# Optimization experiments

Measured on AMD Instinct MI355X. Metric: run time of the kernel, lower is better.

Reference implementation:

```python
import jax, jax.numpy as jnp
import numpy as np


def _layernorm(x, g, b, eps=1e-6):
    mu = jnp.mean(x, -1, keepdims=True)
    var = jnp.var(x, -1, keepdims=True)
    return (x - mu) * jax.lax.rsqrt(var + eps) * g + b


def _rope_interleave(x, cos, sin):
    # de-interleave pairs (x0,x1),(x2,x3),... -> [evens | odds]  (matches
    # torch view(..., d//2, 2).transpose(-1,-2).reshape(..., d))
    x = jnp.concatenate([x[..., 0::2], x[..., 1::2]], axis=-1)
    d = x.shape[-1]
    x1, x2 = x[..., : d // 2], x[..., d // 2 :]
    rot = jnp.concatenate([-x2, x1], axis=-1)
    return x * cos + rot * sin


def setup_inputs() -> dict:
    key = jax.random.key(0)
    k = jax.random.split(key, 6)
    T, H, D, R, HID, QLR, K = 2048, 32, 128, 64, 4096, 1536, 256
    hidden_states = jax.random.normal(k[0], (1, T, HID), jnp.float32)
    q_latent = jax.random.normal(k[1], (1, T, QLR), jnp.float32)
    wq_b = jax.random.normal(k[2], (QLR, H * D), jnp.float32) * 0.02
    wk = jax.random.normal(k[3], (HID, D), jnp.float32) * 0.02
    w_proj = jax.random.normal(k[4], (HID, H), jnp.float32) * 0.02
    k_gamma = jnp.ones((D,), jnp.float32)
    k_beta = jnp.zeros((D,), jnp.float32)
    # real rotary cos/sin tables for the 64-dim rope slice
    pos = jnp.arange(T, dtype=jnp.float32)
    inv_freq = 1.0 / (10000.0 ** (jnp.arange(0, R, 2, dtype=jnp.float32) / R))
    freqs = jnp.outer(pos, inv_freq)
    emb = jnp.concatenate([freqs, freqs], axis=-1)  # [T, R]
    cos, sin = jnp.cos(emb), jnp.sin(emb)
    ks = jnp.zeros((T,), jnp.int32)
    ke = jnp.arange(1, T + 1, dtype=jnp.int32)  # causal: keys [0, t]
    return dict(hidden_states=hidden_states, q_latent=q_latent, ks=ks, ke=ke,
                cos=cos, sin=sin, wq_b=wq_b, wk=wk, k_gamma=k_gamma,
                k_beta=k_beta, w_proj=w_proj, index_topk=K)


def reference(hidden_states, q_latent, ks, ke, cos, sin, wq_b, wk,
              k_gamma, k_beta, w_proj, index_topk):
    T = hidden_states.shape[1]
    H = w_proj.shape[1]
    D = wk.shape[1]
    R = cos.shape[-1]
    weight_scale = (D ** -0.5) * (H ** -0.5)

    q = (q_latent[0] @ wq_b).reshape(T, H, D)              # [T,H,D]
    k = _layernorm(hidden_states[0] @ wk, k_gamma, k_beta)  # [T,D]
    w = hidden_states[0] @ w_proj                           # [T,H]

    q_pe = _rope_interleave(q[..., :R], cos[:, None, :], sin[:, None, :])
    k_pe = _rope_interleave(k[..., :R], cos, sin)
    q = jnp.concatenate([q_pe, q[..., R:]], axis=-1)
    k = jnp.concatenate([k_pe, k[..., R:]], axis=-1)

    # lightning-indexer score: I[t,s] = sum_h w[t,h] * relu(q[t,h] . k[s])
    scores = jnp.einsum('thd,sd->ths', q, k)                # [T,H,S]
    scores = jnp.einsum('ths,th->ts', jax.nn.relu(scores), w) * weight_scale

    j = jnp.arange(T)
    mask = (j[None, :] >= ks[:, None]) & (j[None, :] < ke[:, None])
    scores = jnp.where(mask, scores, -1e30)
    values, idx = jax.lax.top_k(scores, index_topk)
    return idx.reshape(1, T, 1, index_topk), values
```

## Files before the change

### kernel.cpp

```cpp
#include <hip/hip_runtime.h>
#include <cstdint>

typedef unsigned short u16;
typedef unsigned int   u32;
typedef unsigned long long u64;

typedef short bf16x8 __attribute__((ext_vector_type(8)));
typedef float f32x4  __attribute__((ext_vector_type(4)));
typedef u16   u16x8  __attribute__((ext_vector_type(8)));

__device__ __forceinline__ u16 f2b(float f){
  u32 u = __float_as_uint(f);
  u += 0x7FFFu + ((u >> 16) & 1u);
  return (u16)(u >> 16);
}
__device__ __forceinline__ float b2f(u16 h){ return __uint_as_float(((u32)h) << 16); }
__device__ __forceinline__ u32 fkey(float f){
  u32 u = __float_as_uint(f);
  return u ^ ((u & 0x80000000u) ? 0xFFFFFFFFu : 0x80000000u);
}
__device__ __forceinline__ float unkey(u32 k){
  u32 u = (k & 0x80000000u) ? (k ^ 0x80000000u) : ~k;
  return __uint_as_float(u);
}
__device__ __forceinline__ void gload16(const void* g, void* l){
  __builtin_amdgcn_global_load_lds(
      reinterpret_cast<const __attribute__((address_space(1))) char*>(reinterpret_cast<uintptr_t>(g)),
      reinterpret_cast<__attribute__((address_space(3))) char*>(reinterpret_cast<uintptr_t>(l)),
      16, 0, 0);
}

__global__ __launch_bounds__(256) void k_init(const int* __restrict__ ke, int* __restrict__ list){
  __shared__ int km[64];
  int tid = threadIdx.x;
  if (tid < 64){
    int m = 0;
    for (int j = 0; j < 32; j++) m = max(m, ke[tid * 32 + j]);
    km[tid] = m;
  }
  __syncthreads();
  if (tid < 8){
    int x = tid, n = 0;
    for (int j0 = 0; j0 < 8; j0++){
      int tb = j0 * 8 + x;
      int kmax = km[tb];
      for (int sb = 0; sb < 16; sb++){
        if (sb * 128 < kmax){
          list[n * 8 + x] = tb * 32 + sb * 2 + 0; n++;
          list[n * 8 + x] = tb * 32 + sb * 2 + 1; n++;
        }
      }
    }
    for (; n < 256; n++) list[n * 8 + x] = -1;
  }
}

__global__ __launch_bounds__(256) void k_cvt(const float* __restrict__ in, u16* __restrict__ out, int n8){
  int i = blockIdx.x * 256 + threadIdx.x;
  if (i >= n8) return;
  const float4* p = (const float4*)in + (size_t)i * 2;
  float4 a = p[0], b = p[1];
  u16x8 v;
  v[0]=f2b(a.x); v[1]=f2b(a.y); v[2]=f2b(a.z); v[3]=f2b(a.w);
  v[4]=f2b(b.x); v[5]=f2b(b.y); v[6]=f2b(b.z); v[7]=f2b(b.w);
  *((u16x8*)out + i) = v;
}

__global__ __launch_bounds__(256) void k_tcvt(const float* __restrict__ in, u16* __restrict__ out, int R, int C){
  __shared__ float tile[32][33];
  int c0 = blockIdx.x * 32, r0 = blockIdx.y * 32;
  int tx = threadIdx.x & 31, ty = threadIdx.x >> 5;
  for (int i = 0; i < 4; i++){
    int r = ty * 4 + i;
    tile[r][tx] = in[(size_t)(r0 + r) * C + c0 + tx];
  }
  __syncthreads();
  for (int i = 0; i < 4; i++){
    int c = ty * 4 + i;
    out[(size_t)(c0 + c) * R + r0 + tx] = f2b(tile[tx][c]);
  }
}

__global__ __launch_bounds__(256) void k_wct(const float* __restrict__ wk, const float* __restrict__ wp, u16* __restrict__ out){
  __shared__ float tile[32][33];
  int c0 = blockIdx.x * 32, i0 = blockIdx.y * 32;
  int tx = threadIdx.x & 31, ty = threadIdx.x >> 5;
  for (int j = 0; j < 4; j++){
    int i = i0 + ty * 4 + j;
    int c = c0 + tx;
    float v = 0.f;
    if (c < 128) v = wk[(size_t)i * 128 + c];
    else if (c < 160) v = wp[(size_t)i * 32 + (c - 128)];
    tile[ty * 4 + j][tx] = v;
  }
  __syncthreads();
  for (int j = 0; j < 4; j++){
    int c = c0 + ty * 4 + j;
    out[(size_t)c * 4096 + i0 + tx] = f2b(tile[tx][ty * 4 + j]);
  }
}

__global__ __launch_bounds__(256) void k_gemm_kw(const float* __restrict__ A, const u16* __restrict__ B, float* __restrict__ Cp){
  const int Kd = 4096, NC = 192;
  __shared__ float As[128 * 64];
  __shared__ u16 Bs[64 * 64];
  int lin = blockIdx.x;
  int xcd = lin & 7, idx = lin >> 3;
  int nb = idx % 3, pz = idx / 3;
  int p = xcd + 8 * pz;
  int m0 = (p & 15) * 128;
  int kt0 = (p >> 4) * 512;
  int n0 = nb * 64;
  float* C = Cp + (size_t)(p >> 4) * 2048 * NC;
  int tid = threadIdx.x, lane = tid & 63, wid = tid >> 6;
  int wm = wid * 32;
  f32x4 acc[2][4] = {};
  for (int kt = kt0; kt < kt0 + 512; kt += 64){
    for (int c = tid; c < 2048; c += 256){
      int row = c >> 4, slot = (c & 15) ^ (row & 7);
      gload16(A + (size_t)(m0 + row) * Kd + kt + slot * 4, (float*)As + (size_t)c * 4);
    }
    for (int c = tid; c < 512; c += 256){
      int row = c >> 3, slot = (c & 7) ^ (row & 7);
      gload16(B + (size_t)(n0 + row) * Kd + kt + slot * 8, (u16*)Bs + (size_t)c * 8);
    }
    __syncthreads();
    for (int kk = 0; kk < 2; kk++){
      bf16x8 af[2], bfr[4];
      for (int i = 0; i < 2; i++){
        int row = wm + i * 16 + (lane & 15);
        int c0 = kk * 8 + (lane >> 4) * 2;
        f32x4 lo = *(const f32x4*)&As[row * 64 + ((c0)     ^ (row & 7)) * 4];
        f32x4 hi = *(const f32x4*)&As[row * 64 + ((c0 + 1) ^ (row & 7)) * 4];
        bf16x8 t;
        t[0]=(short)f2b(lo[0]); t[1]=(short)f2b(lo[1]); t[2]=(short)f2b(lo[2]); t[3]=(short)f2b(lo[3]);
        t[4]=(short)f2b(hi[0]); t[5]=(short)f2b(hi[1]); t[6]=(short)f2b(hi[2]); t[7]=(short)f2b(hi[3]);
        af[i] = t;
      }
      for (int j = 0; j < 4; j++){
        int row = j * 16 + (lane & 15);
        int slot = (kk * 4 + (lane >> 4)) ^ (row & 7);
        bfr[j] = *(const bf16x8*)&Bs[row * 64 + slot * 8];
      }
      for (int i = 0; i < 2; i++)
        for (int j = 0; j < 4; j++)
          acc[i][j] = __builtin_amdgcn_mfma_f32_16x16x32_bf16(af[i], bfr[j], acc[i][j], 0, 0, 0);
    }
    __syncthreads();
  }
  for (int i = 0; i < 2; i++)
    for (int j = 0; j < 4; j++){
      int row = m0 + wm + i * 16 + ((lane >> 4) * 4);
      int col = n0 + j * 16 + (lane & 15);
      for (int r = 0; r < 4; r++)
        C[(size_t)(row + r) * NC + col] = acc[i][j][r];
    }
}

__global__ __launch_bounds__(256) void k_lnrope(const float* __restrict__ kwp, const float* __restrict__ gamma,
                                                const float* __restrict__ beta, const float* __restrict__ cosp,
                                                const float* __restrict__ sinp, u16* __restrict__ krot,
                                                float* __restrict__ wfin){
  const size_t ZS = (size_t)2048 * 192;
  int row = blockIdx.x * 4 + (threadIdx.x >> 6);
  int lane = threadIdx.x & 63;
  const float* x = kwp + (size_t)row * 192;
  float2 v = {0.f, 0.f};
  for (int z = 0; z < 8; z++){
    float2 p = *(const float2*)&x[z * ZS + lane * 2];
    v.x += p.x; v.y += p.y;
  }
  float s = v.x + v.y, ss = v.x * v.x + v.y * v.y;
  for (int o = 32; o; o >>= 1){ s += __shfl_xor(s, o); ss += __shfl_xor(ss, o); }
  float mu = s * (1.f / 128.f);
  float var = ss * (1.f / 128.f) - mu * mu;
  float rs = rsqrtf(var + 1e-6f);
  float y0 = (v.x - mu) * rs * gamma[lane * 2]     + beta[lane * 2];
  float y1 = (v.y - mu) * rs * gamma[lane * 2 + 1] + beta[lane * 2 + 1];
  u16* out = krot + (size_t)row * 128;
  if (lane < 32){
    float c = cosp[(size_t)row * 64 + lane], sn = sinp[(size_t)row * 64 + lane];
    out[lane]      = f2b(y0 * c - y1 * sn);
    out[lane + 32] = f2b(y1 * c + y0 * sn);
    float wsum = 0.f;
    for (int z = 0; z < 8; z++) wsum += x[z * ZS + 128 + lane];
    wfin[(size_t)row * 32 + lane] = wsum;
  } else {
    out[lane * 2]     = f2b(y0);
    out[lane * 2 + 1] = f2b(y1);
  }
}

__global__ __launch_bounds__(256) void k_gemm_q(const u16* __restrict__ A, const u16* __restrict__ B,
                                                const float* __restrict__ cosp, const float* __restrict__ sinp,
                                                u16* __restrict__ C){
  const int N = 4096, Kd = 1536;
  __shared__ u16 As[128 * 64];
  __shared__ u16 Bs[128 * 64];
  int linb = blockIdx.x;
  int xcd = linb & 7, loc = linb >> 3;
  int n0 = (xcd * 4 + (loc >> 4)) * 128;
  int m0 = (loc & 15) * 128;
  int tid = threadIdx.x, lane = tid & 63, wid = tid >> 6;
  int wm = (wid >> 1) * 64, wn = (wid & 1) * 64;
  f32x4 acc[4][4] = {};
  for (int kt = 0; kt < Kd; kt += 64){
    for (int c = tid; c < 1024; c += 256){
      int row = c >> 3, slot = (c & 7) ^ (row & 7);
      gload16(A + (size_t)(m0 + row) * Kd + kt + slot * 8, (u16*)As + (size_t)c * 8);
      gload16(B + (size_t)(n0 + row) * Kd + kt + slot * 8, (u16*)Bs + (size_t)c * 8);
    }
    __syncthreads();
    for (int kk = 0; kk < 2; kk++){
      bf16x8 af[4], bfr[4];
      for (int i = 0; i < 4; i++){
        int rowa = wm + i * 16 + (lane & 15);
        int rowb = wn + i * 16 + (lane & 15);
        int sa = (kk * 4 + (lane >> 4)) ^ (rowa & 7);
        int sbx = (kk * 4 + (lane >> 4)) ^ (rowb & 7);
        af[i]  = *(const bf16x8*)&As[rowa * 64 + sa * 8];
        bfr[i] = *(const bf16x8*)&Bs[rowb * 64 + sbx * 8];
      }
      for (int i = 0; i < 4; i++)
        for (int j = 0; j < 4; j++)
          acc[i][j] = __builtin_amdgcn_mfma_f32_16x16x32_bf16(af[i], bfr[j], acc[i][j], 0, 0, 0);
    }
    __syncthreads();
  }
  if (wn == 0){
    int l = lane & 15;
    int base = lane & 48;
    int sl = base + ((2 * l) & 15);
    for (int i = 0; i < 4; i++){
      int rowb = m0 + wm + i * 16 + ((lane >> 4) * 4);
      f32x4 ne[4];
      for (int j = 0; j < 4; j++){
        int jj = j & 1;
        for (int r = 0; r < 4; r++){
          float eA = __shfl(acc[i][2 * jj][r],     sl);
          float eB = __shfl(acc[i][2 * jj + 1][r], sl);
          float oA = __shfl(acc[i][2 * jj][r],     sl + 1);
          float oB = __shfl(acc[i][2 * jj + 1][r], sl + 1);
          float e = (l >= 8) ? eB : eA;
          float o = (l >= 8) ? oB : oA;
          int row = rowb + r;
          int d = j * 16 + l;
          float c = cosp[(size_t)row * 64 + d];
          float s = sinp[(size_t)row * 64 + d];
          ne[j][r] = (j < 2) ? (e * c - o * s) : (o * c + e * s);
        }
      }
      for (int j = 0; j < 4; j++) acc[i][j] = ne[j];
    }
  }
  for (int i = 0; i < 4; i++)
    for (int j = 0; j < 4; j++){
      int row = m0 + wm + i * 16 + ((lane >> 4) * 4);
      int col = n0 + wn + j * 16 + (lane & 15);
      for (int r = 0; r < 4; r++)
        C[(size_t)(row + r) * N + col] = f2b(acc[i][j][r]);
    }
}

__global__ __launch_bounds__(256, 4) void k_scores(const u16* __restrict__ q, const u16* __restrict__ krot,
                                                   const float* __restrict__ wfin, const int* __restrict__ list,
                                                   float* __restrict__ S0, float* __restrict__ S1){
  __shared__ u16 Bs[128 * 128];
  __shared__ float Ws[16][32];
  int e = list[blockIdx.x];
  if (e < 0) return;
  int tb = e >> 5, sb = (e >> 1) & 15, hgrp = e & 1;
  int t0 = tb * 32, s0 = sb * 128;
  int tid = threadIdx.x, lane = tid & 63, wid = tid >> 6;
  int wr = wid >> 1, wc = wid & 1;

  for (int c = tid; c < 2048; c += 256){
    int row = c >> 4, slot = (c & 15) ^ (row & 7);
    gload16(krot + (size_t)(s0 + row) * 128 + slot * 8, (u16*)Bs + (size_t)c * 8);
  }
  for (int i = tid; i < 512; i += 256){
    int h = i >> 5, r = i & 31;
    Ws[h][r] = wfin[(size_t)(t0 + r) * 32 + hgrp * 16 + h];
  }
  __syncthreads();

  bf16x8 bfr[4][4];
#pragma unroll
  for (int j = 0; j < 4; j++)
#pragma unroll
    for (int kc = 0; kc < 4; kc++){
      int row = wc * 64 + j * 16 + (lane & 15);
      int slot = (kc * 4 + (lane >> 4)) ^ (row & 7);
      bfr[j][kc] = *(const bf16x8*)&Bs[row * 128 + slot * 8];
    }

  f32x4 acc[4] = {};
  const u16* qbase = q + ((size_t)t0 + wr * 16 + (lane & 15)) * 4096 + (size_t)hgrp * 16 * 128 + (lane >> 4) * 8;
  int rbase = wr * 16 + ((lane >> 4) * 4);
#pragma unroll
  for (int h = 0; h < 16; h++){
    bf16x8 af[4];
#pragma unroll
    for (int kc = 0; kc < 4; kc++)
      af[kc] = *(const bf16x8*)&qbase[h * 128 + kc * 32];
    f32x4 ah[4] = {};
#pragma unroll
    for (int kc = 0; kc < 4; kc++)
#pragma unroll
      for (int j = 0; j < 4; j++)
        ah[j] = __builtin_amdgcn_mfma_f32_16x16x32_bf16(af[kc], bfr[j][kc], ah[j], 0, 0, 0);
#pragma unroll
    for (int r = 0; r < 4; r++){
      float wv = Ws[h][rbase + r];
#pragma unroll
      for (int j = 0; j < 4; j++)
        acc[j][r] += fmaxf(ah[j][r], 0.f) * wv;
    }
  }
  float* Sp = hgrp ? S1 : S0;
#pragma unroll
  for (int j = 0; j < 4; j++){
    int col = s0 + wc * 64 + j * 16 + (lane & 15);
#pragma unroll
    for (int r = 0; r < 4; r++)
      Sp[(size_t)(t0 + rbase + r) * 2048 + col] = acc[j][r];
  }
}

__global__ __launch_bounds__(256) void k_topk(const float* __restrict__ S0, const float* __restrict__ S1,
                                              const int* __restrict__ ktp, const int* __restrict__ ksv,
                                              const int* __restrict__ ke, float* __restrict__ out){
  int t = blockIdx.x;
  int T = gridDim.x;
  const float* r0 = S0 + (size_t)t * 2048;
  const float* r1 = S1 + (size_t)t * 2048;
  __shared__ u32 keys[2048];
  __shared__ u32 hist[256];
  __shared__ u32 ssum[256];
  __shared__ u32 sb, srem;
  __shared__ u32 wtot[8];
  __shared__ int selIdx[256];
  __shared__ u32 baseGt, baseTie;
  __shared__ u64 skey[256];
  int tid = threadIdx.x;
  int K = ktp[0]; if (K > 256) K = 256;
  int ket = ke[t]; if (ket < 0) ket = 0; if (ket > 2048) ket = 2048;
  int kst = ksv[t]; if (kst < 0) kst = 0;
  int limit = (ket + 255) & ~255;
  if (limit < 256) limit = 256;
  if (limit > 2048) limit = 2048;
  const u32 kneg = fkey(-1e30f);
  const float scale = 0.015625f;
  for (int i4 = tid; i4 < (limit >> 2); i4 += 256){
    int base = i4 * 4;
    float4 a = ((const float4*)r0)[i4];
    float4 b = ((const float4*)r1)[i4];
    float v0 = (a.x + b.x) * scale, v1 = (a.y + b.y) * scale;
    float v2 = (a.z + b.z) * scale, v3 = (a.w + b.w) * scale;
    keys[base + 0] = (base + 0 >= kst && base + 0 < ket) ? fkey(v0) : kneg;
    keys[base + 1] = (base + 1 >= kst && base + 1 < ket) ? fkey(v1) : kneg;
    keys[base + 2] = (base + 2 >= kst && base + 2 < ket) ? fkey(v2) : kneg;
    keys[base + 3] = (base + 3 >= kst && base + 3 < ket) ? fkey(v3) : kneg;
  }
  __syncthreads();
  if (limit > K){
    u32 prefix = 0, pmask = 0, rem = (u32)K;
    for (int p = 3; p >= 0; p--){
      int sh = p * 8;
      hist[tid] = 0;
      __syncthreads();
      for (int i = tid; i < limit; i += 256){
        u32 u = keys[i];
        if ((u & pmask) == prefix) atomicAdd(&hist[(u >> sh) & 255], 1u);
      }
      __syncthreads();
      ssum[tid] = hist[tid];
      __syncthreads();
      for (int off = 1; off < 256; off <<= 1){
        u32 add = (tid + off < 256) ? ssum[tid + off] : 0u;
        __syncthreads();
        ssum[tid] += add;
        __syncthreads();
      }
      u32 mine = ssum[tid];
      u32 above = (tid == 255) ? 0u : ssum[tid + 1];
      if (mine >= rem && above < rem){ sb = (u32)tid; srem = rem - above; }
      __syncthreads();
      prefix |= (sb << sh);
      pmask |= (255u << sh);
      rem = srem;
      __syncthreads();
    }
    u32 thr = prefix;
    int G = K - (int)rem;
    if (tid == 0){ baseGt = 0; baseTie = 0; }
    __syncthreads();
    int nch = limit >> 8;
    for (int ch = 0; ch < nch; ch++){
      int i = ch * 256 + tid;
      u32 u = keys[i];
      bool gt = (u > thr), tie = (u == thr);
      u64 bg = __ballot(gt), bt = __ballot(tie);
      int lane = tid & 63, w = tid >> 6;
      if (lane == 0){ wtot[w] = (u32)__popcll(bg); wtot[4 + w] = (u32)__popcll(bt); }
      __syncthreads();
      u32 og = baseGt, ot = baseTie;
      for (int ww = 0; ww < w; ww++){ og += wtot[ww]; ot += wtot[4 + ww]; }
      og += (u32)__popcll(bg & ((1ull << lane) - 1ull));
      ot += (u32)__popcll(bt & ((1ull << lane) - 1ull));
      if (gt) selIdx[og] = i;
      else if (tie && ot < rem) selIdx[G + ot] = i;
      __syncthreads();
      if (tid == 0){
        for (int ww = 0; ww < 4; ww++){ baseGt += wtot[ww]; baseTie += wtot[4 + ww]; }
      }
      __syncthreads();
    }
    if (tid < K){
      int si = selIdx[tid];
      u32 u = keys[si];
      skey[tid] = ((u64)(~u) << 32) | (u32)si;
    } else {
      skey[tid] = ~0ull;
    }
  } else {
    if (tid < K) skey[tid] = ((u64)(~keys[tid]) << 32) | (u32)tid;
    else skey[tid] = ~0ull;
  }
  __syncthreads();
  for (int size = 2; size <= 256; size <<= 1){
    for (int stride = size >> 1; stride > 0; stride >>= 1){
      int p = tid ^ stride;
      if (p > tid){
        bool up = ((tid & size) == 0);
        u64 a = skey[tid], b = skey[p];
        if ((a > b) == up){ skey[tid] = b; skey[p] = a; }
      }
      __syncthreads();
    }
  }
  if (tid < K){
    u64 sk = skey[tid];
    int idx = (int)(u32)(sk & 0xFFFFFFFFu);
    float val = unkey(~(u32)(sk >> 32));
    out[(size_t)t * K + tid] = (float)idx;
    out[(size_t)T * K + (size_t)t * K + tid] = val;
  }
}

extern "C" void kernel_launch(void* const* d_in, const int* in_sizes, int n_in,
                              void* d_out, int out_size, void* d_ws, size_t ws_size,
                              hipStream_t stream){
  const float* hs   = (const float*)d_in[0];
  const float* ql   = (const float*)d_in[1];
  const int*   ks   = (const int*)  d_in[2];
  const int*   ke   = (const int*)  d_in[3];
  const float* cosp = (const float*)d_in[4];
  const float* sinp = (const float*)d_in[5];
  const float* wqb  = (const float*)d_in[6];
  const float* wk   = (const float*)d_in[7];
  const float* kg   = (const float*)d_in[8];
  const float* kb   = (const float*)d_in[9];
  const float* wp   = (const float*)d_in[10];
  const int*   ktp  = (const int*)  d_in[11];

  char* w = (char*)d_ws;
  u16* qlb = (u16*)w;  w += (size_t)2048 * 1536 * 2;
  u16* wqT = (u16*)w;  w += (size_t)4096 * 1536 * 2;
  u16* wct = (u16*)w;  w += (size_t)192 * 4096 * 2;
  u16* qb  = (u16*)w;  w += (size_t)2048 * 4096 * 2;
  float* kwp = (float*)w; w += (size_t)8 * 2048 * 192 * 4;
  float* wfin = (float*)w; w += (size_t)2048 * 32 * 4;
  u16* krt = (u16*)w;  w += (size_t)2048 * 128 * 2;
  float* S0 = (float*)w; w += (size_t)2048 * 2048 * 4;
  int* list = (int*)w;  w += 2048 * 4;
  float* S1 = (float*)d_ws;

  hipLaunchKernelGGL(k_init, dim3(1), dim3(256), 0, stream, ke, list);
  hipLaunchKernelGGL(k_cvt, dim3(1536), dim3(256), 0, stream, ql, qlb, 393216);
  hipLaunchKernelGGL(k_tcvt, dim3(128, 48), dim3(256), 0, stream, wqb, wqT, 1536, 4096);
  hipLaunchKernelGGL(k_wct, dim3(6, 128), dim3(256), 0, stream, wk, wp, wct);
  hipLaunchKernelGGL(k_gemm_kw, dim3(384), dim3(256), 0, stream, hs, wct, kwp);
  hipLaunchKernelGGL(k_lnrope, dim3(512), dim3(256), 0, stream, kwp, kg, kb, cosp, sinp, krt, wfin);
  hipLaunchKernelGGL(k_gemm_q, dim3(512), dim3(256), 0, stream, qlb, wqT, cosp, sinp, qb);
  hipLaunchKernelGGL(k_scores, dim3(2048), dim3(256), 0, stream, qb, krt, wfin, list, S0, S1);
  hipLaunchKernelGGL(k_topk, dim3(2048), dim3(256), 0, stream, S0, S1, ktp, ks, ke, (float*)d_out);
}
```

Measured before the change: 158.5 us.

## Split score heads into four groups and store bf16 partial scores

The scores kernel now handles 8 heads per block instead of 16, so the launch grows from 2048 to 4096 blocks to give more parallel work on the causal tile list. The per-head-group partial sums are stored as bf16 in four buffers instead of two fp32 buffers, which keeps the total bytes written the same. The top-k kernel reads and sums the four bf16 partials. The trade-offs are that each K tile is loaded into shared memory twice as often, and that bf16 rounding of partial sums can change the top-k ordering among near-equal scores.

```diff
diff --git a/kernel.cpp b/kernel.cpp
--- a/kernel.cpp
+++ b/kernel.cpp
@@ -46,12 +46,11 @@
       int kmax = km[tb];
       for (int sb = 0; sb < 16; sb++){
         if (sb * 128 < kmax){
-          list[n * 8 + x] = tb * 32 + sb * 2 + 0; n++;
-          list[n * 8 + x] = tb * 32 + sb * 2 + 1; n++;
+          for (int hg = 0; hg < 4; hg++){ list[n * 8 + x] = tb * 64 + sb * 4 + hg; n++; }
         }
       }
     }
-    for (; n < 256; n++) list[n * 8 + x] = -1;
+    for (; n < 512; n++) list[n * 8 + x] = -1;
   }
 }
 
@@ -264,12 +263,13 @@
 
 __global__ __launch_bounds__(256, 4) void k_scores(const u16* __restrict__ q, const u16* __restrict__ krot,
                                                    const float* __restrict__ wfin, const int* __restrict__ list,
-                                                   float* __restrict__ S0, float* __restrict__ S1){
+                                                   u16* __restrict__ Sb0, u16* __restrict__ Sb1,
+                                                   u16* __restrict__ Sb2, u16* __restrict__ Sb3){
   __shared__ u16 Bs[128 * 128];
-  __shared__ float Ws[16][32];
+  __shared__ float Ws[8][32];
   int e = list[blockIdx.x];
   if (e < 0) return;
-  int tb = e >> 5, sb = (e >> 1) & 15, hgrp = e & 1;
+  int tb = e >> 6, sb = (e >> 2) & 15, hg = e & 3;
   int t0 = tb * 32, s0 = sb * 128;
   int tid = threadIdx.x, lane = tid & 63, wid = tid >> 6;
   int wr = wid >> 1, wc = wid & 1;
@@ -278,9 +278,9 @@
     int row = c >> 4, slot = (c & 15) ^ (row & 7);
     gload16(krot + (size_t)(s0 + row) * 128 + slot * 8, (u16*)Bs + (size_t)c * 8);
   }
-  for (int i = tid; i < 512; i += 256){
-    int h = i >> 5, r = i & 31;
-    Ws[h][r] = wfin[(size_t)(t0 + r) * 32 + hgrp * 16 + h];
+  if (tid < 256){
+    int h = tid >> 5, r = tid & 31;
+    if (h < 8) Ws[h][r] = wfin[(size_t)(t0 + r) * 32 + hg * 8 + h];
   }
   __syncthreads();
 
@@ -295,10 +295,10 @@
     }
 
   f32x4 acc[4] = {};
-  const u16* qbase = q + ((size_t)t0 + wr * 16 + (lane & 15)) * 4096 + (size_t)hgrp * 16 * 128 + (lane >> 4) * 8;
+  const u16* qbase = q + ((size_t)t0 + wr * 16 + (lane & 15)) * 4096 + (size_t)hg * 8 * 128 + (lane >> 4) * 8;
   int rbase = wr * 16 + ((lane >> 4) * 4);
 #pragma unroll
-  for (int h = 0; h < 16; h++){
+  for (int h = 0; h < 8; h++){
     bf16x8 af[4];
 #pragma unroll
     for (int kc = 0; kc < 4; kc++)
@@ -317,23 +317,26 @@
         acc[j][r] += fmaxf(ah[j][r], 0.f) * wv;
     }
   }
-  float* Sp = hgrp ? S1 : S0;
+  u16* Sp = (hg == 0) ? Sb0 : (hg == 1) ? Sb1 : (hg == 2) ? Sb2 : Sb3;
 #pragma unroll
   for (int j = 0; j < 4; j++){
     int col = s0 + wc * 64 + j * 16 + (lane & 15);
 #pragma unroll
     for (int r = 0; r < 4; r++)
-      Sp[(size_t)(t0 + rbase + r) * 2048 + col] = acc[j][r];
-  }
-}
-
-__global__ __launch_bounds__(256) void k_topk(const float* __restrict__ S0, const float* __restrict__ S1,
+      Sp[(size_t)(t0 + rbase + r) * 2048 + col] = f2b(acc[j][r]);
+  }
+}
+
+__global__ __launch_bounds__(256) void k_topk(const u16* __restrict__ Sb0, const u16* __restrict__ Sb1,
+                                              const u16* __restrict__ Sb2, const u16* __restrict__ Sb3,
                                               const int* __restrict__ ktp, const int* __restrict__ ksv,
                                               const int* __restrict__ ke, float* __restrict__ out){
   int t = blockIdx.x;
   int T = gridDim.x;
-  const float* r0 = S0 + (size_t)t * 2048;
-  const float* r1 = S1 + (size_t)t * 2048;
+  const u16* r0 = Sb0 + (size_t)t * 2048;
+  const u16* r1 = Sb1 + (size_t)t * 2048;
+  const u16* r2 = Sb2 + (size_t)t * 2048;
+  const u16* r3 = Sb3 + (size_t)t * 2048;
   __shared__ u32 keys[2048];
   __shared__ u32 hist[256];
   __shared__ u32 ssum[256];
@@ -351,16 +354,18 @@
   if (limit > 2048) limit = 2048;
   const u32 kneg = fkey(-1e30f);
   const float scale = 0.015625f;
-  for (int i4 = tid; i4 < (limit >> 2); i4 += 256){
-    int base = i4 * 4;
-    float4 a = ((const float4*)r0)[i4];
-    float4 b = ((const float4*)r1)[i4];
-    float v0 = (a.x + b.x) * scale, v1 = (a.y + b.y) * scale;
-    float v2 = (a.z + b.z) * scale, v3 = (a.w + b.w) * scale;
-    keys[base + 0] = (base + 0 >= kst && base + 0 < ket) ? fkey(v0) : kneg;
-    keys[base + 1] = (base + 1 >= kst && base + 1 < ket) ? fkey(v1) : kneg;
-    keys[base + 2] = (base + 2 >= kst && base + 2 < ket) ? fkey(v2) : kneg;
-    keys[base + 3] = (base + 3 >= kst && base + 3 < ket) ? fkey(v3) : kneg;
+  for (int i8 = tid; i8 < (limit >> 3); i8 += 256){
+    int base = i8 * 8;
+    u16x8 a = ((const u16x8*)r0)[i8];
+    u16x8 b = ((const u16x8*)r1)[i8];
+    u16x8 c = ((const u16x8*)r2)[i8];
+    u16x8 d = ((const u16x8*)r3)[i8];
+#pragma unroll
+    for (int e = 0; e < 8; e++){
+      int i = base + e;
+      float v = (b2f(a[e]) + b2f(b[e]) + b2f(c[e]) + b2f(d[e])) * scale;
+      keys[i] = (i >= kst && i < ket) ? fkey(v) : kneg;
+    }
   }
   __syncthreads();
   if (limit > K){
@@ -472,9 +477,11 @@
   float* kwp = (float*)w; w += (size_t)8 * 2048 * 192 * 4;
   float* wfin = (float*)w; w += (size_t)2048 * 32 * 4;
   u16* krt = (u16*)w;  w += (size_t)2048 * 128 * 2;
-  float* S0 = (float*)w; w += (size_t)2048 * 2048 * 4;
-  int* list = (int*)w;  w += 2048 * 4;
-  float* S1 = (float*)d_ws;
+  u16* Sb0 = (u16*)w;  w += (size_t)2048 * 2048 * 2;
+  u16* Sb1 = (u16*)w;  w += (size_t)2048 * 2048 * 2;
+  int* list = (int*)w; w += 4096 * 4;
+  u16* Sb2 = (u16*)d_ws;
+  u16* Sb3 = (u16*)((char*)d_ws + (size_t)2048 * 2048 * 2);
 
   hipLaunchKernelGGL(k_init, dim3(1), dim3(256), 0, stream, ke, list);
   hipLaunchKernelGGL(k_cvt, dim3(1536), dim3(256), 0, stream, ql, qlb, 393216);
@@ -483,6 +490,6 @@
   hipLaunchKernelGGL(k_gemm_kw, dim3(384), dim3(256), 0, stream, hs, wct, kwp);
   hipLaunchKernelGGL(k_lnrope, dim3(512), dim3(256), 0, stream, kwp, kg, kb, cosp, sinp, krt, wfin);
   hipLaunchKernelGGL(k_gemm_q, dim3(512), dim3(256), 0, stream, qlb, wqT, cosp, sinp, qb);
-  hipLaunchKernelGGL(k_scores, dim3(2048), dim3(256), 0, stream, qb, krt, wfin, list, S0, S1);
-  hipLaunchKernelGGL(k_topk, dim3(2048), dim3(256), 0, stream, S0, S1, ktp, ks, ke, (float*)d_out);
-}
+  hipLaunchKernelGGL(k_scores, dim3(4096), dim3(256), 0, stream, qb, krt, wfin, list, Sb0, Sb1, Sb2, Sb3);
+  hipLaunchKernelGGL(k_topk, dim3(2048), dim3(256), 0, stream, Sb0, Sb1, Sb2, Sb3, ktp, ks, ke, (float*)d_out);
+}
```

Measured after the change: 257.8 us. 62.7% more time.
